# Optimization experiments

Measured on AMD Instinct MI355X. Metric: run time of the kernel, lower is better.

## Reference

```python
import jax, jax.numpy as jnp
import numpy as np

EPS = 1e-9


def _feature_map(x, W, b):
    # nn.Linear: x @ W.T + b, then concat[exp(z), exp(-z)] on last dim
    z = jnp.einsum('bnd,ed->bne', x, W) + b
    return jnp.concatenate([jnp.exp(z), jnp.exp(-z)], axis=-1)  # [b, n, 2d]


def setup_inputs() -> dict:
    key = jax.random.key(0)
    ks = jax.random.split(key, 6)
    b, n, d = 4, 4096, 64
    s = 1.0 / np.sqrt(d)
    hidden = jax.random.normal(ks[0], (b, n, d), dtype=jnp.float32)
    # Hedgehog init is identity + zero bias; add tiny noise so grads are generic
    eye = jnp.eye(d, dtype=jnp.float32)
    Wq_mlp = eye + 0.02 * jax.random.normal(ks[1], (d, d), dtype=jnp.float32)
    Wk_mlp = eye + 0.02 * jax.random.normal(ks[2], (d, d), dtype=jnp.float32)
    bq_mlp = jnp.zeros((d,), dtype=jnp.float32)
    bk_mlp = jnp.zeros((d,), dtype=jnp.float32)
    Wq_base = s * jax.random.normal(ks[3], (d, d), dtype=jnp.float32)
    Wk_base = s * jax.random.normal(ks[4], (d, d), dtype=jnp.float32)
    return {"hidden_states": hidden, "Wq_mlp": Wq_mlp, "bq_mlp": bq_mlp,
            "Wk_mlp": Wk_mlp, "bk_mlp": bk_mlp,
            "Wq_base": Wq_base, "Wk_base": Wk_base}


def reference(hidden_states, Wq_mlp, bq_mlp, Wk_mlp, bk_mlp, Wq_base, Wk_base):
    d = hidden_states.shape[-1]
    # frozen base attention -> true_attn [b, n, n]
    qb = jnp.einsum('bnd,ed->bne', hidden_states, Wq_base)
    kb = jnp.einsum('bnd,ed->bne', hidden_states, Wk_base)
    true_attn = jax.nn.softmax(
        jnp.einsum('bmd,bnd->bmn', qb, kb) / jnp.sqrt(jnp.float32(d)), axis=-1)
    # hedgehog feature maps -> [b, n, 2d]
    q = _feature_map(hidden_states, Wq_mlp, bq_mlp)
    k = _feature_map(hidden_states, Wk_mlp, bk_mlp)
    # quadratic scores + softmax (note: linear-attention form is NOT used here)
    scores = jnp.einsum('bmd,bnd->bmn', q, k)
    pred_attn = jax.nn.softmax(scores, axis=-1)
    # soft-label cross entropy (KD loss)
    loss = jnp.mean(jnp.sum(-true_attn * jnp.log(pred_attn + EPS), axis=-1))
    return (loss, pred_attn, true_attn)
```

## Files before the change

kernel.cpp:

```cpp
#include <hip/hip_runtime.h>
#include <hip/hip_bf16.h>
#include <math.h>


#define B 4
#define N 4096
#define D 64
#define NROWS (B * N)
#define ATTN_ELEMS ((size_t)B * N * N)

typedef __attribute__((ext_vector_type(8))) short short8;
typedef __attribute__((ext_vector_type(4))) float float4v;

typedef unsigned short ushort_t;

__device__ __forceinline__ void split_bf16(float x, ushort_t& hi, ushort_t& lo) {
  __hip_bfloat16 h = __float2bfloat16(x);
  float r = x - __bfloat162float(h);
  __hip_bfloat16 l = __float2bfloat16(r);
  hi = *(ushort_t*)&h;
  lo = *(ushort_t*)&l;
}

__device__ __forceinline__ void gload_lds16(const ushort_t* g, ushort_t* l) {
  __builtin_amdgcn_global_load_lds(
      (const __attribute__((address_space(1))) unsigned int*)g,
      (__attribute__((address_space(3))) unsigned int*)l, 16, 0, 0);
}

#define PR 32

__global__ __launch_bounds__(256, 2) void proj_kernel(
    const float* __restrict__ hidden,
    const float* __restrict__ Wq_mlp, const float* __restrict__ bq_mlp,
    const float* __restrict__ Wk_mlp, const float* __restrict__ bk_mlp,
    const float* __restrict__ Wq_base, const float* __restrict__ Wk_base,
    ushort_t* __restrict__ ws) {
  ushort_t* qbh = ws;
  ushort_t* qbl = ws + 1048576;
  ushort_t* kbh = ws + 2097152;
  ushort_t* kbl = ws + 3145728;
  ushort_t* qfh = ws + 4194304;
  ushort_t* qfl = ws + 6291456;
  ushort_t* kfh = ws + 8388608;
  ushort_t* kfl = ws + 10485760;

  __shared__ float wt[4][64 * 64];
  __shared__ float hs[PR][64];

  const int tid = threadIdx.x;
  const int r0 = blockIdx.x * PR;

  {
    const float* Wm[4] = {Wq_base, Wk_base, Wq_mlp, Wk_mlp};
#pragma unroll
    for (int m = 0; m < 4; ++m)
      for (int idx = tid; idx < 4096; idx += 256) {
        const int e = idx >> 6, d = idx & 63;
        wt[m][d * 64 + (e ^ (d & 31))] = Wm[m][idx];
      }
  }
  for (int idx = tid; idx < PR * 64; idx += 256)
    hs[idx >> 6][idx & 63] = hidden[(size_t)r0 * 64 + idx];
  __syncthreads();

  const int e = tid & 63;
  const int g0 = (tid >> 6) * (PR / 4);

  float aqb[PR / 4], akb[PR / 4], zq[PR / 4], zk[PR / 4];
  const float bq = bq_mlp[e], bk = bk_mlp[e];
#pragma unroll
  for (int g = 0; g < PR / 4; ++g) {
    aqb[g] = 0.f; akb[g] = 0.f; zq[g] = bq; zk[g] = bk;
  }

#pragma unroll 8
  for (int d = 0; d < 64; ++d) {
    const int wi = d * 64 + (e ^ (d & 31));
    const float w0 = wt[0][wi];
    const float w1 = wt[1][wi];
    const float w2 = wt[2][wi];
    const float w3 = wt[3][wi];
#pragma unroll
    for (int g = 0; g < PR / 4; ++g) {
      const float hd = hs[g0 + g][d];
      aqb[g] += hd * w0;
      akb[g] += hd * w1;
      zq[g] += hd * w2;
      zk[g] += hd * w3;
    }
  }

#pragma unroll
  for (int g = 0; g < PR / 4; ++g) {
    const int row = r0 + g0 + g;
    const size_t rb = (size_t)row * D + e;
    const size_t rf = (size_t)row * 2 * D + e;
    ushort_t hi, lo;
    split_bf16(aqb[g], hi, lo);        qbh[rb] = hi; qbl[rb] = lo;
    split_bf16(akb[g], hi, lo);        kbh[rb] = hi; kbl[rb] = lo;
    split_bf16(expf(zq[g]), hi, lo);   qfh[rf] = hi; qfl[rf] = lo;
    split_bf16(expf(-zq[g]), hi, lo);  qfh[rf + D] = hi; qfl[rf + D] = lo;
    split_bf16(expf(zk[g]), hi, lo);   kfh[rf] = hi; kfl[rf] = lo;
    split_bf16(expf(-zk[g]), hi, lo);  kfh[rf + D] = hi; kfl[rf + D] = lo;
  }
}

__global__ __launch_bounds__(256, 2) void scores_kernel(
    const ushort_t* __restrict__ ws, float* __restrict__ out) {
  const ushort_t* qbh = ws;
  const ushort_t* qbl = ws + 1048576;
  const ushort_t* kbh = ws + 2097152;
  const ushort_t* kbl = ws + 3145728;
  const ushort_t* qfh = ws + 4194304;
  const ushort_t* qfl = ws + 6291456;
  const ushort_t* kfh = ws + 8388608;
  const ushort_t* kfl = ws + 10485760;

  __shared__ ushort_t sAh[128 * 64];
  __shared__ ushort_t sAl[128 * 64];
  __shared__ ushort_t sBh[128 * 64];
  __shared__ ushort_t sBl[128 * 64];

  const int bt = blockIdx.z;
  const int f = blockIdx.x + 32 * blockIdx.y;
  const int nf = (f & 7) * 128 + (f >> 3);
  const int m0 = (nf >> 5) * 128;
  const int n0 = (nf & 31) * 128;

  const int tid = threadIdx.x;
  const int lane = tid & 63;
  const int w = tid >> 6;
  const int qr = w >> 1, qc = w & 1;
  const int fr = lane & 15;
  const int quad = lane >> 4;

  const int srow = lane >> 3;
  const int sunit = (lane & 7) ^ srow;

  const size_t rowb = (size_t)bt * N;
  float* pred = out + 1;
  float* tru  = out + 1 + ATTN_ELEMS;

#pragma unroll
  for (int phase = 0; phase < 2; ++phase) {
    const ushort_t* Ah = phase ? qfh : qbh;
    const ushort_t* Al = phase ? qfl : qbl;
    const ushort_t* Bh = phase ? kfh : kbh;
    const ushort_t* Bl = phase ? kfl : kbl;
    const int Krow = phase ? 128 : 64;
    const int nchunk = Krow / 64;
    const float scale = phase ? 1.0f : 0.125f;
    float* dst = phase ? pred : tru;

    float4v acc[4][4];
#pragma unroll
    for (int i = 0; i < 4; ++i)
#pragma unroll
      for (int j = 0; j < 4; ++j) acc[i][j] = (float4v)0.f;

    for (int ck = 0; ck < nchunk; ++ck) {
      const int kc = ck * 64;
      __syncthreads();
#pragma unroll
      for (int j = 0; j < 4; ++j) {
        const int chunk = j * 4 + w;
        const int r = chunk * 8 + srow;
        const int loff = chunk * 512;
        const size_t gA = (size_t)(rowb + m0 + r) * Krow + kc + sunit * 8;
        const size_t gB = (size_t)(rowb + n0 + r) * Krow + kc + sunit * 8;
        gload_lds16(Ah + gA, &sAh[loff]);
        gload_lds16(Al + gA, &sAl[loff]);
        gload_lds16(Bh + gB, &sBh[loff]);
        gload_lds16(Bl + gB, &sBl[loff]);
      }
      __syncthreads();

#pragma unroll
      for (int kk = 0; kk < 2; ++kk) {
        short8 ah[4], al[4], bh[4], bl[4];
        const int u8 = ((kk * 4 + quad) ^ (fr & 7)) * 8;
#pragma unroll
        for (int t = 0; t < 4; ++t) {
          const int offA = (qr * 64 + t * 16 + fr) * 64 + u8;
          const int offB = (qc * 64 + t * 16 + fr) * 64 + u8;
          ah[t] = *(const short8*)&sAh[offA];
          al[t] = *(const short8*)&sAl[offA];
          bh[t] = *(const short8*)&sBh[offB];
          bl[t] = *(const short8*)&sBl[offB];
        }
#pragma unroll
        for (int tm = 0; tm < 4; ++tm)
#pragma unroll
          for (int tn = 0; tn < 4; ++tn) {
            acc[tm][tn] = __builtin_amdgcn_mfma_f32_16x16x32_bf16(
                ah[tm], bh[tn], acc[tm][tn], 0, 0, 0);
            acc[tm][tn] = __builtin_amdgcn_mfma_f32_16x16x32_bf16(
                ah[tm], bl[tn], acc[tm][tn], 0, 0, 0);
            acc[tm][tn] = __builtin_amdgcn_mfma_f32_16x16x32_bf16(
                al[tm], bh[tn], acc[tm][tn], 0, 0, 0);
          }
      }
    }

#pragma unroll
    for (int tm = 0; tm < 4; ++tm) {
      const int rbase = m0 + qr * 64 + tm * 16 + quad * 4;
#pragma unroll
      for (int tn = 0; tn < 4; ++tn) {
        const int c = n0 + qc * 64 + tn * 16 + fr;
        float4v v = acc[tm][tn];
#pragma unroll
        for (int reg = 0; reg < 4; ++reg)
          dst[(rowb + rbase + reg) * N + c] = v[reg] * scale;
      }
    }
  }
}

__device__ __forceinline__ float block_reduce(float v, bool is_max, float* red) {
#pragma unroll
  for (int o = 32; o > 0; o >>= 1) {
    float other = __shfl_down(v, o);
    v = is_max ? fmaxf(v, other) : (v + other);
  }
  int w = threadIdx.x >> 6;
  __syncthreads();
  if ((threadIdx.x & 63) == 0) red[w] = v;
  __syncthreads();
  return is_max ? fmaxf(fmaxf(red[0], red[1]), fmaxf(red[2], red[3]))
                : (red[0] + red[1] + red[2] + red[3]);
}

__global__ __launch_bounds__(256) void softmax_loss_kernel(
    float* __restrict__ out, float* __restrict__ partials) {
  const size_t r = blockIdx.x;
  float* pred = out + 1 + r * N;
  float* tru  = out + 1 + ATTN_ELEMS + r * N;
  const int tid = threadIdx.x;

  __shared__ float red[4];

  float lt[16], lp[16];
#pragma unroll
  for (int i = 0; i < 16; ++i) {
    lt[i] = tru[tid + 256 * i];
    lp[i] = pred[tid + 256 * i];
  }

  float mt_ = -INFINITY, mp_ = -INFINITY;
#pragma unroll
  for (int i = 0; i < 16; ++i) {
    mt_ = fmaxf(mt_, lt[i]);
    mp_ = fmaxf(mp_, lp[i]);
  }
  const float MT = block_reduce(mt_, true, red);
  const float MP = block_reduce(mp_, true, red);

  float st = 0.f, sp = 0.f;
#pragma unroll
  for (int i = 0; i < 16; ++i) {
    lt[i] = expf(lt[i] - MT);
    st += lt[i];
    lp[i] = expf(lp[i] - MP);
    sp += lp[i];
  }
  const float ST = block_reduce(st, false, red);
  const float SP = block_reduce(sp, false, red);
  const float it_ = 1.f / ST, ip_ = 1.f / SP;

  float lloss = 0.f;
#pragma unroll
  for (int i = 0; i < 16; ++i) {
    float t = lt[i] * it_;
    float p = lp[i] * ip_;
    tru[tid + 256 * i] = t;
    pred[tid + 256 * i] = p;
    lloss -= t * logf(p + 1e-9f);
  }
  lloss = block_reduce(lloss, false, red);
  if (tid == 0) partials[r] = lloss;
}

__global__ __launch_bounds__(256) void reduce_loss_kernel(
    const float* __restrict__ partials, float* __restrict__ out) {
  const int tid = threadIdx.x;
  __shared__ float red[4];
  float s = 0.f;
  for (int i = tid; i < NROWS; i += 256) s += partials[i];
  s = block_reduce(s, false, red);
  if (tid == 0) out[0] = s * (1.0f / (float)NROWS);
}

extern "C" void kernel_launch(void* const* d_in, const int* in_sizes, int n_in,
                              void* d_out, int out_size, void* d_ws, size_t ws_size,
                              hipStream_t stream) {
  const float* hidden  = (const float*)d_in[0];
  const float* Wq_mlp  = (const float*)d_in[1];
  const float* bq_mlp  = (const float*)d_in[2];
  const float* Wk_mlp  = (const float*)d_in[3];
  const float* bk_mlp  = (const float*)d_in[4];
  const float* Wq_base = (const float*)d_in[5];
  const float* Wk_base = (const float*)d_in[6];
  float* out = (float*)d_out;
  ushort_t* ws = (ushort_t*)d_ws;
  float* partials = (float*)(ws + 12582912);

  proj_kernel<<<NROWS / PR, 256, 0, stream>>>(hidden, Wq_mlp, bq_mlp, Wk_mlp,
                                              bk_mlp, Wq_base, Wk_base, ws);
  scores_kernel<<<dim3(32, 32, B), 256, 0, stream>>>(ws, out);
  softmax_loss_kernel<<<NROWS, 256, 0, stream>>>(out, partials);
  reduce_loss_kernel<<<1, 256, 0, stream>>>(partials, out);
}
```

Baseline: 898.7 us.

## Compute softmax row stats in a separate pass and fuse normalization into score write

After: 828.8 us. -7.8%, faster.

```diff
diff --git a/kernel.cpp b/kernel.cpp
--- a/kernel.cpp
+++ b/kernel.cpp
@@ -8,6 +8,7 @@
 #define D 64
 #define NROWS (B * N)
 #define ATTN_ELEMS ((size_t)B * N * N)
+#define FSTAT_BASE 12582912
 
 typedef __attribute__((ext_vector_type(8))) short short8;
 typedef __attribute__((ext_vector_type(4))) float float4v;
@@ -26,6 +27,20 @@
   __builtin_amdgcn_global_load_lds(
       (const __attribute__((address_space(1))) unsigned int*)g,
       (__attribute__((address_space(3))) unsigned int*)l, 16, 0, 0);
+}
+
+__device__ __forceinline__ float block_reduce(float v, bool is_max, float* red) {
+#pragma unroll
+  for (int o = 32; o > 0; o >>= 1) {
+    float other = __shfl_down(v, o);
+    v = is_max ? fmaxf(v, other) : (v + other);
+  }
+  int w = threadIdx.x >> 6;
+  __syncthreads();
+  if ((threadIdx.x & 63) == 0) red[w] = v;
+  __syncthreads();
+  return is_max ? fmaxf(fmaxf(red[0], red[1]), fmaxf(red[2], red[3]))
+                : (red[0] + red[1] + red[2] + red[3]);
 }
 
 #define PR 32
@@ -106,8 +121,8 @@
   }
 }
 
-__global__ __launch_bounds__(256, 2) void scores_kernel(
-    const ushort_t* __restrict__ ws, float* __restrict__ out) {
+__global__ __launch_bounds__(256) void stats_kernel(
+    const ushort_t* __restrict__ ws, float* __restrict__ fst) {
   const ushort_t* qbh = ws;
   const ushort_t* qbl = ws + 1048576;
   const ushort_t* kbh = ws + 2097152;
@@ -117,10 +132,185 @@
   const ushort_t* kfh = ws + 8388608;
   const ushort_t* kfl = ws + 10485760;
 
+  float* mt_ = fst;
+  float* ist_ = fst + 16384;
+  float* mp_ = fst + 32768;
+  float* isp_ = fst + 49152;
+
+  __shared__ ushort_t sbh[128 * 64];
+  __shared__ ushort_t sbl[128 * 64];
+  __shared__ ushort_t sfh[128 * 128];
+  __shared__ ushort_t sfl[128 * 128];
+
+  const int bid0 = blockIdx.x;
+  const int bid = (bid0 & 7) * 32 + (bid0 >> 3);
+  const int bt = bid >> 6;
+  const int m0 = (bid & 63) * 64;
+  const int tid = threadIdx.x;
+  const int w = tid >> 6;
+  const int lane = tid & 63;
+  const int fr = lane & 15;
+  const int quad = lane >> 4;
+  const size_t rowb = (size_t)bt * N;
+
+  const size_t ar = rowb + m0 + w * 16 + fr;
+  short8 ath[2], atl[2], aph[4], apl[4];
+#pragma unroll
+  for (int kk = 0; kk < 2; ++kk) {
+    ath[kk] = *(const short8*)&qbh[ar * 64 + kk * 32 + quad * 8];
+    atl[kk] = *(const short8*)&qbl[ar * 64 + kk * 32 + quad * 8];
+  }
+#pragma unroll
+  for (int kk = 0; kk < 4; ++kk) {
+    aph[kk] = *(const short8*)&qfh[ar * 128 + kk * 32 + quad * 8];
+    apl[kk] = *(const short8*)&qfl[ar * 128 + kk * 32 + quad * 8];
+  }
+
+  const int sr8 = lane >> 3, su8 = (lane & 7) ^ (lane >> 3);
+  const int r4 = lane >> 4, u16 = lane & 15;
+
+  float m_t[4], s_t[4], m_p[4], s_p[4];
+#pragma unroll
+  for (int r = 0; r < 4; ++r) {
+    m_t[r] = -INFINITY; s_t[r] = 0.f;
+    m_p[r] = -INFINITY; s_p[r] = 0.f;
+  }
+
+  for (int c = 0; c < 32; ++c) {
+    const int n0 = c * 128;
+    __syncthreads();
+#pragma unroll
+    for (int j = 0; j < 4; ++j) {
+      const int g = j * 4 + w;
+      const size_t grow = rowb + n0 + g * 8 + sr8;
+      gload_lds16(kbh + grow * 64 + su8 * 8, &sbh[g * 512]);
+      gload_lds16(kbl + grow * 64 + su8 * 8, &sbl[g * 512]);
+    }
+#pragma unroll
+    for (int j = 0; j < 8; ++j) {
+      const int g = j * 4 + w;
+      const int su = u16 ^ ((g & 1) * 4 + r4);
+      const size_t grow = rowb + n0 + g * 4 + r4;
+      gload_lds16(kfh + grow * 128 + su * 8, &sfh[g * 512]);
+      gload_lds16(kfl + grow * 128 + su * 8, &sfl[g * 512]);
+    }
+    __syncthreads();
+
+    float4v acct[8];
+#pragma unroll
+    for (int tn = 0; tn < 8; ++tn) acct[tn] = (float4v)0.f;
+#pragma unroll
+    for (int tn = 0; tn < 8; ++tn) {
+      const int brow = tn * 16 + fr;
+#pragma unroll
+      for (int kk = 0; kk < 2; ++kk) {
+        const int u = ((kk * 4 + quad) ^ (fr & 7)) * 8;
+        short8 bh = *(const short8*)&sbh[brow * 64 + u];
+        short8 bl = *(const short8*)&sbl[brow * 64 + u];
+        acct[tn] = __builtin_amdgcn_mfma_f32_16x16x32_bf16(ath[kk], bh, acct[tn], 0, 0, 0);
+        acct[tn] = __builtin_amdgcn_mfma_f32_16x16x32_bf16(ath[kk], bl, acct[tn], 0, 0, 0);
+        acct[tn] = __builtin_amdgcn_mfma_f32_16x16x32_bf16(atl[kk], bh, acct[tn], 0, 0, 0);
+      }
+    }
+#pragma unroll
+    for (int r = 0; r < 4; ++r) {
+      float vm = m_t[r];
+      float v[8];
+#pragma unroll
+      for (int tn = 0; tn < 8; ++tn) { v[tn] = acct[tn][r] * 0.125f; vm = fmaxf(vm, v[tn]); }
+      float ss = s_t[r] * expf(m_t[r] - vm);
+#pragma unroll
+      for (int tn = 0; tn < 8; ++tn) ss += expf(v[tn] - vm);
+      m_t[r] = vm; s_t[r] = ss;
+    }
+
+    float4v accp[8];
+#pragma unroll
+    for (int tn = 0; tn < 8; ++tn) accp[tn] = (float4v)0.f;
+#pragma unroll
+    for (int tn = 0; tn < 8; ++tn) {
+      const int brow = tn * 16 + fr;
+#pragma unroll
+      for (int kk = 0; kk < 4; ++kk) {
+        const int u = ((kk * 4 + quad) ^ (fr & 7)) * 8;
+        short8 bh = *(const short8*)&sfh[brow * 128 + u];
+        short8 bl = *(const short8*)&sfl[brow * 128 + u];
+        accp[tn] = __builtin_amdgcn_mfma_f32_16x16x32_bf16(aph[kk], bh, accp[tn], 0, 0, 0);
+        accp[tn] = __builtin_amdgcn_mfma_f32_16x16x32_bf16(aph[kk], bl, accp[tn], 0, 0, 0);
+        accp[tn] = __builtin_amdgcn_mfma_f32_16x16x32_bf16(apl[kk], bh, accp[tn], 0, 0, 0);
+      }
+    }
+#pragma unroll
+    for (int r = 0; r < 4; ++r) {
+      float vm = m_p[r];
+      float v[8];
+#pragma unroll
+      for (int tn = 0; tn < 8; ++tn) { v[tn] = accp[tn][r]; vm = fmaxf(vm, v[tn]); }
+      float ss = s_p[r] * expf(m_p[r] - vm);
+#pragma unroll
+      for (int tn = 0; tn < 8; ++tn) ss += expf(v[tn] - vm);
+      m_p[r] = vm; s_p[r] = ss;
+    }
+  }
+
+#pragma unroll
+  for (int r = 0; r < 4; ++r) {
+    {
+      float m = m_t[r], s = s_t[r];
+#pragma unroll
+      for (int o = 1; o < 16; o <<= 1) {
+        float m2 = __shfl_xor(m, o);
+        float s2 = __shfl_xor(s, o);
+        float M = fmaxf(m, m2);
+        s = s * expf(m - M) + s2 * expf(m2 - M);
+        m = M;
+      }
+      if (fr == 0) {
+        const size_t row = rowb + m0 + w * 16 + quad * 4 + r;
+        mt_[row] = m; ist_[row] = 1.f / s;
+      }
+    }
+    {
+      float m = m_p[r], s = s_p[r];
+#pragma unroll
+      for (int o = 1; o < 16; o <<= 1) {
+        float m2 = __shfl_xor(m, o);
+        float s2 = __shfl_xor(s, o);
+        float M = fmaxf(m, m2);
+        s = s * expf(m - M) + s2 * expf(m2 - M);
+        m = M;
+      }
+      if (fr == 0) {
+        const size_t row = rowb + m0 + w * 16 + quad * 4 + r;
+        mp_[row] = m; isp_[row] = 1.f / s;
+      }
+    }
+  }
+}
+
+__global__ __launch_bounds__(256, 2) void scores_write_kernel(
+    const ushort_t* __restrict__ ws, float* __restrict__ out,
+    float* __restrict__ fst) {
+  const ushort_t* qbh = ws;
+  const ushort_t* qbl = ws + 1048576;
+  const ushort_t* kbh = ws + 2097152;
+  const ushort_t* kbl = ws + 3145728;
+  const ushort_t* qfh = ws + 4194304;
+  const ushort_t* qfl = ws + 6291456;
+  const ushort_t* kfh = ws + 8388608;
+  const ushort_t* kfl = ws + 10485760;
+
+  const float* mt_ = fst;
+  const float* ist_ = fst + 16384;
+  const float* mp_ = fst + 32768;
+  const float* isp_ = fst + 49152;
+  float* partials = fst + 65536;
+
   __shared__ ushort_t sAh[128 * 64];
   __shared__ ushort_t sAl[128 * 64];
   __shared__ ushort_t sBh[128 * 64];
   __shared__ ushort_t sBl[128 * 64];
+  __shared__ float red[4];
 
   const int bt = blockIdx.z;
   const int f = blockIdx.x + 32 * blockIdx.y;
@@ -141,6 +331,9 @@
   const size_t rowb = (size_t)bt * N;
   float* pred = out + 1;
   float* tru  = out + 1 + ATTN_ELEMS;
+
+  float4v tsave[4][4];
+  float lloss = 0.f;
 
 #pragma unroll
   for (int phase = 0; phase < 2; ++phase) {
@@ -206,80 +399,37 @@
 #pragma unroll
     for (int tm = 0; tm < 4; ++tm) {
       const int rbase = m0 + qr * 64 + tm * 16 + quad * 4;
+      float mrow[4], isrow[4];
+#pragma unroll
+      for (int reg = 0; reg < 4; ++reg) {
+        const size_t gr = rowb + rbase + reg;
+        mrow[reg]  = phase ? mp_[gr]  : mt_[gr];
+        isrow[reg] = phase ? isp_[gr] : ist_[gr];
+      }
 #pragma unroll
       for (int tn = 0; tn < 4; ++tn) {
         const int c = n0 + qc * 64 + tn * 16 + fr;
         float4v v = acc[tm][tn];
+        float4v pv;
 #pragma unroll
         for (int reg = 0; reg < 4; ++reg)
-          dst[(rowb + rbase + reg) * N + c] = v[reg] * scale;
-      }
-    }
-  }
-}
-
-__device__ __forceinline__ float block_reduce(float v, bool is_max, float* red) {
-#pragma unroll
-  for (int o = 32; o > 0; o >>= 1) {
-    float other = __shfl_down(v, o);
-    v = is_max ? fmaxf(v, other) : (v + other);
-  }
-  int w = threadIdx.x >> 6;
-  __syncthreads();
-  if ((threadIdx.x & 63) == 0) red[w] = v;
-  __syncthreads();
-  return is_max ? fmaxf(fmaxf(red[0], red[1]), fmaxf(red[2], red[3]))
-                : (red[0] + red[1] + red[2] + red[3]);
-}
-
-__global__ __launch_bounds__(256) void softmax_loss_kernel(
-    float* __restrict__ out, float* __restrict__ partials) {
-  const size_t r = blockIdx.x;
-  float* pred = out + 1 + r * N;
-  float* tru  = out + 1 + ATTN_ELEMS + r * N;
-  const int tid = threadIdx.x;
-
-  __shared__ float red[4];
-
-  float lt[16], lp[16];
-#pragma unroll
-  for (int i = 0; i < 16; ++i) {
-    lt[i] = tru[tid + 256 * i];
-    lp[i] = pred[tid + 256 * i];
-  }
-
-  float mt_ = -INFINITY, mp_ = -INFINITY;
-#pragma unroll
-  for (int i = 0; i < 16; ++i) {
-    mt_ = fmaxf(mt_, lt[i]);
-    mp_ = fmaxf(mp_, lp[i]);
-  }
-  const float MT = block_reduce(mt_, true, red);
-  const float MP = block_reduce(mp_, true, red);
-
-  float st = 0.f, sp = 0.f;
-#pragma unroll
-  for (int i = 0; i < 16; ++i) {
-    lt[i] = expf(lt[i] - MT);
-    st += lt[i];
-    lp[i] = expf(lp[i] - MP);
-    sp += lp[i];
-  }
-  const float ST = block_reduce(st, false, red);
-  const float SP = block_reduce(sp, false, red);
-  const float it_ = 1.f / ST, ip_ = 1.f / SP;
-
-  float lloss = 0.f;
-#pragma unroll
-  for (int i = 0; i < 16; ++i) {
-    float t = lt[i] * it_;
-    float p = lp[i] * ip_;
-    tru[tid + 256 * i] = t;
-    pred[tid + 256 * i] = p;
-    lloss -= t * logf(p + 1e-9f);
-  }
+          pv[reg] = expf(v[reg] * scale - mrow[reg]) * isrow[reg];
+#pragma unroll
+        for (int reg = 0; reg < 4; ++reg)
+          dst[(rowb + rbase + reg) * N + c] = pv[reg];
+        if (phase == 0) {
+          tsave[tm][tn] = pv;
+        } else {
+#pragma unroll
+          for (int reg = 0; reg < 4; ++reg)
+            lloss -= tsave[tm][tn][reg] * logf(pv[reg] + 1e-9f);
+        }
+      }
+    }
+  }
+
   lloss = block_reduce(lloss, false, red);
-  if (tid == 0) partials[r] = lloss;
+  if (tid == 0) partials[f + (bt << 10)] = lloss;
 }
 
 __global__ __launch_bounds__(256) void reduce_loss_kernel(
@@ -287,7 +437,7 @@
   const int tid = threadIdx.x;
   __shared__ float red[4];
   float s = 0.f;
-  for (int i = tid; i < NROWS; i += 256) s += partials[i];
+  for (int i = tid; i < 4096; i += 256) s += partials[i];
   s = block_reduce(s, false, red);
   if (tid == 0) out[0] = s * (1.0f / (float)NROWS);
 }
@@ -304,11 +454,11 @@
   const float* Wk_base = (const float*)d_in[6];
   float* out = (float*)d_out;
   ushort_t* ws = (ushort_t*)d_ws;
-  float* partials = (float*)(ws + 12582912);
+  float* fst = (float*)(ws + FSTAT_BASE);
 
   proj_kernel<<<NROWS / PR, 256, 0, stream>>>(hidden, Wq_mlp, bq_mlp, Wk_mlp,
                                               bk_mlp, Wq_base, Wk_base, ws);
-  scores_kernel<<<dim3(32, 32, B), 256, 0, stream>>>(ws, out);
-  softmax_loss_kernel<<<NROWS, 256, 0, stream>>>(out, partials);
-  reduce_loss_kernel<<<1, 256, 0, stream>>>(partials, out);
-}
+  stats_kernel<<<256, 256, 0, stream>>>(ws, fst);
+  scores_write_kernel<<<dim3(32, 32, B), 256, 0, stream>>>(ws, out, fst);
+  reduce_loss_kernel<<<1, 256, 0, stream>>>(fst + 65536, out);
+}
```
